# Kernel optimization log

Hardware: AMD Instinct MI355X
Metric: run time of the kernel (lower is better)

Reference implementation:

```python
import jax, jax.numpy as jnp
import numpy as np

C = 256  # in/feat/out channels
EPS = 1e-5

def layer_norm(x, g, b):
    mu = jnp.mean(x, axis=-1, keepdims=True)
    var = jnp.var(x, axis=-1, keepdims=True)
    return (x - mu) * jax.lax.rsqrt(var + EPS) * g + b

def setup_inputs() -> dict:
    key = jax.random.key(0)
    ks = jax.random.split(key, 16)
    N, K = 16384, 9
    s = 1.0 / np.sqrt(C)
    d = {
        "update_feature": jax.random.normal(ks[0], (N, C), jnp.float32),
        "input_feature": jax.random.normal(ks[1], (N, K, C), jnp.float32),
        "dyn_W": jax.random.uniform(ks[2], (2 * C, C), jnp.float32, -s, s),
        "dyn_b": jnp.zeros((2 * C,), jnp.float32),
        "inp_W": jax.random.uniform(ks[3], (2 * C, C), jnp.float32, -s, s),
        "inp_b": jnp.zeros((2 * C,), jnp.float32),
        "ig_W": jax.random.uniform(ks[4], (C, C), jnp.float32, -s, s),
        "ig_b": jnp.zeros((C,), jnp.float32),
        "ug_W": jax.random.uniform(ks[5], (C, C), jnp.float32, -s, s),
        "ug_b": jnp.zeros((C,), jnp.float32),
        "fc_W": jax.random.uniform(ks[6], (C, C), jnp.float32, -s, s),
        "fc_b": jnp.zeros((C,), jnp.float32),
        "norm_in_g": jnp.ones((C,), jnp.float32), "norm_in_b": jnp.zeros((C,), jnp.float32),
        "norm_out_g": jnp.ones((C,), jnp.float32), "norm_out_b": jnp.zeros((C,), jnp.float32),
        "inorm_in_g": jnp.ones((C,), jnp.float32), "inorm_in_b": jnp.zeros((C,), jnp.float32),
        "inorm_out_g": jnp.ones((C,), jnp.float32), "inorm_out_b": jnp.zeros((C,), jnp.float32),
        "fc_norm_g": jnp.ones((C,), jnp.float32), "fc_norm_b": jnp.zeros((C,), jnp.float32),
    }
    return d

def reference(update_feature, input_feature, dyn_W, dyn_b, inp_W, inp_b,
              ig_W, ig_b, ug_W, ug_b, fc_W, fc_b,
              norm_in_g, norm_in_b, norm_out_g, norm_out_b,
              inorm_in_g, inorm_in_b, inorm_out_g, inorm_out_b,
              fc_norm_g, fc_norm_b):
    uf = update_feature.reshape(-1, C)                     # [N, C]
    N = uf.shape[0]
    params = uf @ dyn_W.T + dyn_b                          # [N, 2C]
    param_in, param_out = params[:, :C], params[:, C:]
    inf = input_feature.reshape(N, -1, C)                  # [N, K, C]
    input_feats = jnp.einsum('nkc,dc->nkd', inf, inp_W) + inp_b  # [N, K, 2C]
    input_in, input_out = input_feats[..., :C], input_feats[..., C:]
    gate_feats = input_in * param_in[:, None, :]           # [N, K, C]
    input_gate = jax.nn.sigmoid(layer_norm(jnp.einsum('nkc,dc->nkd', gate_feats, ig_W) + ig_b, inorm_in_g, inorm_in_b))
    update_gate = jax.nn.sigmoid(layer_norm(jnp.einsum('nkc,dc->nkd', gate_feats, ug_W) + ug_b, norm_in_g, norm_in_b))
    param_out = layer_norm(param_out, norm_out_g, norm_out_b)
    input_out = layer_norm(input_out, inorm_out_g, inorm_out_b)
    features = update_gate * param_out[:, None, :] + input_gate * input_out
    features = jnp.einsum('nkc,dc->nkd', features, fc_W) + fc_b
    features = jax.nn.relu(layer_norm(features, fc_norm_g, fc_norm_b))
    return features
```

## Files before the change

### kernel.cpp

```cpp
#include <hip/hip_runtime.h>

#define EPS 1e-5f
#define APITCH 264

typedef __attribute__((ext_vector_type(8))) short bf16x8;
typedef __attribute__((ext_vector_type(4))) float f32x4;
typedef __attribute__((ext_vector_type(2))) float f32x2;

__device__ __forceinline__ unsigned short f2b_rtne(float f) {
  unsigned u = __builtin_bit_cast(unsigned, f);
  u += 0x7fffu + ((u >> 16) & 1u);
  return (unsigned short)(u >> 16);
}
__device__ __forceinline__ unsigned cvt_pk(float lo, float hi) {
  unsigned r;
  asm("v_cvt_pk_bf16_f32 %0, %1, %2" : "=v"(r) : "v"(lo), "v"(hi));
  return r;
}
__device__ __forceinline__ float bhalf(unsigned pk, int hi) {
  unsigned u = hi ? (pk & 0xffff0000u) : (pk << 16);
  return __builtin_bit_cast(float, u);
}
__device__ __forceinline__ int div9(int r) {
  return (int)(__umulhi((unsigned)r, 954437177u) >> 1);
}
__device__ __forceinline__ float fsig(float x) {
  return __builtin_amdgcn_rcpf(1.f + __expf(-x));
}

__device__ __forceinline__ f32x2 pk_add(f32x2 a, f32x2 b) {
  f32x2 d; asm("v_pk_add_f32 %0, %1, %2" : "=v"(d) : "v"(a), "v"(b)); return d;
}
__device__ __forceinline__ f32x2 pk_mul(f32x2 a, f32x2 b) {
  f32x2 d; asm("v_pk_mul_f32 %0, %1, %2" : "=v"(d) : "v"(a), "v"(b)); return d;
}
__device__ __forceinline__ f32x2 pk_fma(f32x2 a, f32x2 b, f32x2 c) {
  f32x2 d; asm("v_pk_fma_f32 %0, %1, %2, %3" : "=v"(d) : "v"(a), "v"(b), "v"(c)); return d;
}
__device__ __forceinline__ f32x2 ld2(const float* p) { return *(const f32x2*)p; }

template <int CTRL>
__device__ __forceinline__ float dppadd(float v) {
  int x = __builtin_amdgcn_update_dpp(0, __builtin_bit_cast(int, v), CTRL, 0xf, 0xf, true);
  return v + __builtin_bit_cast(float, x);
}
__device__ __forceinline__ float dpp_reduce16(float v) {
  v = dppadd<0xB1>(v);
  v = dppadd<0x4E>(v);
  v = dppadd<0x124>(v);
  v = dppadd<0x128>(v);
  return v;
}

__global__ void k_cvt_all(const float* __restrict__ dynW, const float* __restrict__ inpW,
                          const float* __restrict__ igW, const float* __restrict__ ugW,
                          const float* __restrict__ fcW, unsigned short* __restrict__ dst) {
  int i = blockIdx.x * blockDim.x + threadIdx.x;
  const float* src; int off; int perm;
  if (i < 131072)      { src = dynW; off = i;          perm = 0; }
  else if (i < 262144) { src = inpW; off = i - 131072; perm = 0; }
  else if (i < 327680) { src = igW;  off = i - 262144; perm = 1; }
  else if (i < 393216) { src = ugW;  off = i - 327680; perm = 1; }
  else                 { src = fcW;  off = i - 393216; perm = 1; }
  int j = off & 7, lane = (off >> 3) & 63, kk = (off >> 9) & 7, ct = off >> 12;
  int row = ct * 16 + (lane & 15);
  int p = kk * 32 + (lane >> 4) * 8 + j;
  int col = perm ? ((p & ~63) + (p & 3) * 16 + ((p >> 2) & 15)) : p;
  dst[i] = f2b_rtne(src[row * 256 + col]);
}


__device__ __forceinline__ void gemmQ(const short* src,
                                      const unsigned short* __restrict__ W,
                                      f32x4 (&acc)[4][2],
                                      int wv, int lane, int lr, int lh) {
#pragma unroll
  for (int q = 0; q < 4; q++) {
    const unsigned short* Wp = W + ((wv * 4 + q) << 12) + lane * 8;
    bf16x8 b[8];
#pragma unroll
    for (int kk = 0; kk < 8; kk++) b[kk] = *(const bf16x8*)&Wp[kk * 512];
    int zoff = 0;
    asm volatile("" : "+v"(zoff));
    const short* ap = src + zoff;
    bf16x8 a[8];
#pragma unroll
    for (int kk = 0; kk < 8; kk++)
      a[kk] = *(const bf16x8*)&ap[lr * APITCH + kk * 32 + lh * 8];
    acc[q][0] = (f32x4){0.f, 0.f, 0.f, 0.f};
#pragma unroll
    for (int kk = 0; kk < 8; kk++)
      acc[q][0] = __builtin_amdgcn_mfma_f32_16x16x32_bf16(a[kk], b[kk], acc[q][0], 0, 0, 0);
#pragma unroll
    for (int kk = 0; kk < 8; kk++)
      a[kk] = *(const bf16x8*)&ap[(16 + lr) * APITCH + kk * 32 + lh * 8];
    acc[q][1] = (f32x4){0.f, 0.f, 0.f, 0.f};
#pragma unroll
    for (int kk = 0; kk < 8; kk++)
      acc[q][1] = __builtin_amdgcn_mfma_f32_16x16x32_bf16(a[kk], b[kk], acc[q][1], 0, 0, 0);
  }
}

__device__ __forceinline__ void statsW(const f32x4 (&acc)[4][2], const f32x2 (&b42)[4],
                                       float* sP, float* qP, int wv, int lr, int lh) {
#pragma unroll
  for (int rh = 0; rh < 2; rh++)
#pragma unroll
    for (int p = 0; p < 2; p++) {
      f32x2 s2 = (f32x2){0.f, 0.f}, q2 = (f32x2){0.f, 0.f};
#pragma unroll
      for (int q = 0; q < 4; q++) {
        f32x2 a2 = (f32x2){acc[q][rh][2 * p], acc[q][rh][2 * p + 1]};
        f32x2 t = pk_add(a2, b42[q]);
        s2 = pk_add(s2, t);
        q2 = pk_fma(t, t, q2);
      }
      float s0 = dpp_reduce16(s2[0]);
      float s1 = dpp_reduce16(s2[1]);
      float q0 = dpp_reduce16(q2[0]);
      float q1 = dpp_reduce16(q2[1]);
      if (lr == 0) {
        int r = rh * 16 + lh * 4 + 2 * p;
        sP[wv * 32 + r] = s0;  sP[wv * 32 + r + 1] = s1;
        qP[wv * 32 + r] = q0;  qP[wv * 32 + r + 1] = q1;
      }
    }
}
__device__ __forceinline__ void statsR(const float* sP, const float* qP,
                                       f32x2 (&nmu)[2][2], f32x2 (&rv)[2][2], int lh) {
#pragma unroll
  for (int rh = 0; rh < 2; rh++)
#pragma unroll
    for (int p = 0; p < 2; p++) {
      int r = rh * 16 + lh * 4 + 2 * p;
      f32x2 S = pk_add(pk_add(ld2(sP + r), ld2(sP + 32 + r)),
                       pk_add(ld2(sP + 64 + r), ld2(sP + 96 + r)));
      f32x2 Q = pk_add(pk_add(ld2(qP + r), ld2(qP + 32 + r)),
                       pk_add(ld2(qP + 64 + r), ld2(qP + 96 + r)));
      float m0 = S[0] * (1.f / 256.f), m1 = S[1] * (1.f / 256.f);
      nmu[rh][p] = (f32x2){-m0, -m1};
      rv[rh][p] = (f32x2){rsqrtf(Q[0] * (1.f / 256.f) - m0 * m0 + EPS),
                          rsqrtf(Q[1] * (1.f / 256.f) - m1 * m1 + EPS)};
    }
}

__global__ __launch_bounds__(256) void k_main(
    const float* __restrict__ inf,
    const unsigned short* __restrict__ inpWf, const float* __restrict__ inpb,
    const unsigned short* __restrict__ igWf, const float* __restrict__ igb,
    const unsigned short* __restrict__ ugWf, const float* __restrict__ ugb,
    const unsigned short* __restrict__ fcWf, const float* __restrict__ fcb,
    const float* __restrict__ nig, const float* __restrict__ nib,
    const float* __restrict__ iig, const float* __restrict__ iib,
    const float* __restrict__ iog, const float* __restrict__ iob,
    const float* __restrict__ fng, const float* __restrict__ fnb,
    const float* __restrict__ param_in, const float* __restrict__ param_out_ln,
    float* __restrict__ out) {
  __shared__ short aT[32 * APITCH];
  __shared__ short gT[32 * APITCH];
  __shared__ float sP[2][128], qP[2][128];

  const int t = threadIdx.x;
  const int wv = t >> 6, lane = t & 63, lr = lane & 15, lh = lane >> 4;
  const int cb = wv * 64;
  const int r0 = blockIdx.x * 32;

#pragma unroll
  for (int j = 0; j < 8; j++) {
    const int idx4 = j * 256 + t;
    const int row = idx4 >> 6;
    const int c4 = (idx4 & 63) << 2;
    const float4 v = *(const float4*)&inf[(size_t)(r0 + row) * 256 + c4];
    uint2 pk;
    pk.x = cvt_pk(v.x, v.y);
    pk.y = cvt_pk(v.z, v.w);
    *(uint2*)&aT[row * APITCH + c4] = pk;
  }
  __syncthreads();

  f32x4 acc[4][2];
  f32x2 b42[4], ga2[4], be2[4], nmu[2][2], rv[2][2];
  unsigned gio[4][2][2];

  gemmQ(aT, inpWf, acc, wv, lane, lr, lh);
#pragma unroll
  for (int q = 0; q < 4; q++) { float b = inpb[cb + q * 16 + lr]; b42[q] = (f32x2){b, b}; }
#pragma unroll
  for (int rh = 0; rh < 2; rh++)
#pragma unroll
    for (int p = 0; p < 2; p++) {
      const int rrA = rh * 16 + lh * 4 + 2 * p;
      const float* pin0 = param_in + (size_t)div9(r0 + rrA) * 256;
      const float* pin1 = param_in + (size_t)div9(r0 + rrA + 1) * 256;
      float gAv[4], gBv[4];
#pragma unroll
      for (int q = 0; q < 4; q++) {
        f32x2 a2 = (f32x2){acc[q][rh][2 * p], acc[q][rh][2 * p + 1]};
        f32x2 tt = pk_add(a2, b42[q]);
        gAv[q] = tt[0] * pin0[cb + q * 16 + lr];
        gBv[q] = tt[1] * pin1[cb + q * 16 + lr];
      }
      uint2 pkA, pkB;
      pkA.x = cvt_pk(gAv[0], gAv[1]); pkA.y = cvt_pk(gAv[2], gAv[3]);
      pkB.x = cvt_pk(gBv[0], gBv[1]); pkB.y = cvt_pk(gBv[2], gBv[3]);
      *(uint2*)&gT[rrA * APITCH + cb + lr * 4] = pkA;
      *(uint2*)&gT[(rrA + 1) * APITCH + cb + lr * 4] = pkB;
    }

  gemmQ(aT, inpWf + (16 << 12), acc, wv, lane, lr, lh);
#pragma unroll
  for (int q = 0; q < 4; q++) { float b = inpb[256 + cb + q * 16 + lr]; b42[q] = (f32x2){b, b}; }
  statsW(acc, b42, sP[1], qP[1], wv, lr, lh);
  __syncthreads();
  statsR(sP[1], qP[1], nmu, rv, lh);
#pragma unroll
  for (int q = 0; q < 4; q++) {
    float g = iog[cb + q * 16 + lr], e = iob[cb + q * 16 + lr];
    ga2[q] = (f32x2){g, g}; be2[q] = (f32x2){e, e};
  }
#pragma unroll
  for (int q = 0; q < 4; q++)
#pragma unroll
    for (int rh = 0; rh < 2; rh++)
#pragma unroll
      for (int p = 0; p < 2; p++) {
        f32x2 a2 = (f32x2){acc[q][rh][2 * p], acc[q][rh][2 * p + 1]};
        f32x2 tt = pk_add(pk_add(a2, b42[q]), nmu[rh][p]);
        f32x2 v2 = pk_fma(pk_mul(tt, rv[rh][p]), ga2[q], be2[q]);
        gio[q][rh][p] = cvt_pk(v2[0], v2[1]);
      }

  gemmQ(gT, igWf, acc, wv, lane, lr, lh);
#pragma unroll
  for (int q = 0; q < 4; q++) { float b = igb[cb + q * 16 + lr]; b42[q] = (f32x2){b, b}; }
  statsW(acc, b42, sP[0], qP[0], wv, lr, lh);
  __syncthreads();
  statsR(sP[0], qP[0], nmu, rv, lh);
#pragma unroll
  for (int q = 0; q < 4; q++) {
    float g = iig[cb + q * 16 + lr], e = iib[cb + q * 16 + lr];
    ga2[q] = (f32x2){g, g}; be2[q] = (f32x2){e, e};
  }
#pragma unroll
  for (int q = 0; q < 4; q++)
#pragma unroll
    for (int rh = 0; rh < 2; rh++)
#pragma unroll
      for (int p = 0; p < 2; p++) {
        f32x2 a2 = (f32x2){acc[q][rh][2 * p], acc[q][rh][2 * p + 1]};
        f32x2 tt = pk_add(pk_add(a2, b42[q]), nmu[rh][p]);
        f32x2 p2 = pk_fma(pk_mul(tt, rv[rh][p]), ga2[q], be2[q]);
        float g10 = fsig(p2[0]);
        float g11 = fsig(p2[1]);
        unsigned w = gio[q][rh][p];
        gio[q][rh][p] = cvt_pk(g10 * bhalf(w, 0), g11 * bhalf(w, 1));
      }

  gemmQ(gT, ugWf, acc, wv, lane, lr, lh);
#pragma unroll
  for (int q = 0; q < 4; q++) { float b = ugb[cb + q * 16 + lr]; b42[q] = (f32x2){b, b}; }
  statsW(acc, b42, sP[1], qP[1], wv, lr, lh);
  __syncthreads();
  statsR(sP[1], qP[1], nmu, rv, lh);
#pragma unroll
  for (int q = 0; q < 4; q++) {
    float g = nig[cb + q * 16 + lr], e = nib[cb + q * 16 + lr];
    ga2[q] = (f32x2){g, g}; be2[q] = (f32x2){e, e};
  }
#pragma unroll
  for (int rh = 0; rh < 2; rh++)
#pragma unroll
    for (int p = 0; p < 2; p++) {
      const int rrA = rh * 16 + lh * 4 + 2 * p;
      const float* po0 = param_out_ln + (size_t)div9(r0 + rrA) * 256;
      const float* po1 = param_out_ln + (size_t)div9(r0 + rrA + 1) * 256;
      float fA[4], fB[4];
#pragma unroll
      for (int q = 0; q < 4; q++) {
        f32x2 a2 = (f32x2){acc[q][rh][2 * p], acc[q][rh][2 * p + 1]};
        f32x2 tt = pk_add(pk_add(a2, b42[q]), nmu[rh][p]);
        f32x2 u2 = pk_fma(pk_mul(tt, rv[rh][p]), ga2[q], be2[q]);
        float g20 = fsig(u2[0]);
        float g21 = fsig(u2[1]);
        unsigned w = gio[q][rh][p];
        fA[q] = g20 * po0[cb + q * 16 + lr] + bhalf(w, 0);
        fB[q] = g21 * po1[cb + q * 16 + lr] + bhalf(w, 1);
      }
      uint2 pkA, pkB;
      pkA.x = cvt_pk(fA[0], fA[1]); pkA.y = cvt_pk(fA[2], fA[3]);
      pkB.x = cvt_pk(fB[0], fB[1]); pkB.y = cvt_pk(fB[2], fB[3]);
      *(uint2*)&aT[rrA * APITCH + cb + lr * 4] = pkA;
      *(uint2*)&aT[(rrA + 1) * APITCH + cb + lr * 4] = pkB;
    }
  __syncthreads();

  gemmQ(aT, fcWf, acc, wv, lane, lr, lh);
#pragma unroll
  for (int q = 0; q < 4; q++) { float b = fcb[cb + q * 16 + lr]; b42[q] = (f32x2){b, b}; }
  statsW(acc, b42, sP[0], qP[0], wv, lr, lh);
  __syncthreads();
  statsR(sP[0], qP[0], nmu, rv, lh);
#pragma unroll
  for (int q = 0; q < 4; q++) {
    float g = fng[cb + q * 16 + lr], e = fnb[cb + q * 16 + lr];
    ga2[q] = (f32x2){g, g}; be2[q] = (f32x2){e, e};
  }
#pragma unroll
  for (int q = 0; q < 4; q++) {
    const int col = cb + q * 16 + lr;
#pragma unroll
    for (int rh = 0; rh < 2; rh++)
#pragma unroll
      for (int p = 0; p < 2; p++) {
        f32x2 a2 = (f32x2){acc[q][rh][2 * p], acc[q][rh][2 * p + 1]};
        f32x2 tt = pk_add(pk_add(a2, b42[q]), nmu[rh][p]);
        f32x2 v2 = pk_fma(pk_mul(tt, rv[rh][p]), ga2[q], be2[q]);
        const int rrA = r0 + rh * 16 + lh * 4 + 2 * p;
        out[(size_t)rrA * 256 + col] = fmaxf(v2[0], 0.f);
        out[(size_t)(rrA + 1) * 256 + col] = fmaxf(v2[1], 0.f);
      }
  }
}

#define FPITCH 516

__device__ __forceinline__ void red8(float& s, float& q) {
#pragma unroll
  for (int m = 1; m < 8; m <<= 1) { s += __shfl_xor(s, m); q += __shfl_xor(q, m); }
}

__global__ __launch_bounds__(256) void k_params(
    const float* __restrict__ uf, const unsigned short* __restrict__ dynWf,
    const float* __restrict__ dynb, const float* __restrict__ nog,
    const float* __restrict__ nob, float* __restrict__ param_in,
    float* __restrict__ param_out_ln) {
  __shared__ short aT[32 * APITCH];
  __shared__ float fBuf[32 * FPITCH];
  const int t = threadIdx.x;
  const int wv = t >> 6, lane = t & 63, lr = lane & 15, lh = lane >> 4;
  const int r0 = blockIdx.x * 32;
#pragma unroll
  for (int j = 0; j < 8; j++) {
    const int idx4 = j * 256 + t;
    const int row = idx4 >> 6;
    const int c4 = (idx4 & 63) << 2;
    const float4 v = *(const float4*)&uf[(size_t)(r0 + row) * 256 + c4];
    uint2 pk;
    pk.x = cvt_pk(v.x, v.y);
    pk.y = cvt_pk(v.z, v.w);
    *(uint2*)&aT[row * APITCH + c4] = pk;
  }
  __syncthreads();
  bf16x8 a0[8], a1[8];
#pragma unroll
  for (int kk = 0; kk < 8; kk++) {
    a0[kk] = *(const bf16x8*)&aT[lr * APITCH + kk * 32 + lh * 8];
    a1[kk] = *(const bf16x8*)&aT[(16 + lr) * APITCH + kk * 32 + lh * 8];
  }
#pragma unroll 1
  for (int cp = 0; cp < 8; cp++) {
    const int ct = wv * 8 + cp;
    bf16x8 b[8];
#pragma unroll
    for (int kk = 0; kk < 8; kk++)
      b[kk] = *(const bf16x8*)&dynWf[((ct * 8 + kk) * 64 + lane) * 8];
    const float bi = dynb[ct * 16 + lr];
    f32x4 c0 = {0.f, 0.f, 0.f, 0.f}, c1 = c0;
#pragma unroll
    for (int kk = 0; kk < 8; kk++) {
      c0 = __builtin_amdgcn_mfma_f32_16x16x32_bf16(a0[kk], b[kk], c0, 0, 0, 0);
      c1 = __builtin_amdgcn_mfma_f32_16x16x32_bf16(a1[kk], b[kk], c1, 0, 0, 0);
    }
#pragma unroll
    for (int i = 0; i < 4; i++) {
      fBuf[(lh * 4 + i) * FPITCH + ct * 16 + lr] = c0[i] + bi;
      fBuf[(16 + lh * 4 + i) * FPITCH + ct * 16 + lr] = c1[i] + bi;
    }
  }
  __syncthreads();
  const int row = t >> 3, j = t & 7;
  float s = 0.f, q = 0.f;
#pragma unroll
  for (int i = 0; i < 32; i++) {
    float x = fBuf[row * FPITCH + 256 + j + 8 * i];
    s += x; q += x * x;
  }
  red8(s, q);
  const float mu = s * (1.f / 256.f);
  const float rsv = rsqrtf(q * (1.f / 256.f) - mu * mu + EPS);
#pragma unroll 1
  for (int i = 0; i < 32; i++) {
    const int c = j + 8 * i;
    float x = fBuf[row * FPITCH + 256 + c];
    param_out_ln[(size_t)(r0 + row) * 256 + c] = (x - mu) * rsv * nog[c] + nob[c];
  }
#pragma unroll
  for (int jj = 0; jj < 8; jj++) {
    const int idx4 = jj * 256 + t;
    const int rwq = idx4 >> 6;
    const int c4 = (idx4 & 63) << 2;
    float4 v;
    v.x = fBuf[rwq * FPITCH + c4 + 0];
    v.y = fBuf[rwq * FPITCH + c4 + 1];
    v.z = fBuf[rwq * FPITCH + c4 + 2];
    v.w = fBuf[rwq * FPITCH + c4 + 3];
    *(float4*)&param_in[(size_t)(r0 + rwq) * 256 + c4] = v;
  }
}

extern "C" void kernel_launch(void* const* d_in, const int* in_sizes, int n_in,
                              void* d_out, int out_size, void* d_ws, size_t ws_size,
                              hipStream_t stream) {
  const float* uf   = (const float*)d_in[0];
  const float* inf  = (const float*)d_in[1];
  const float* dynW = (const float*)d_in[2];
  const float* dynb = (const float*)d_in[3];
  const float* inpW = (const float*)d_in[4];
  const float* inpb = (const float*)d_in[5];
  const float* igW  = (const float*)d_in[6];
  const float* igb  = (const float*)d_in[7];
  const float* ugW  = (const float*)d_in[8];
  const float* ugb  = (const float*)d_in[9];
  const float* fcW  = (const float*)d_in[10];
  const float* fcb  = (const float*)d_in[11];
  const float* nig  = (const float*)d_in[12];
  const float* nib  = (const float*)d_in[13];
  const float* nog  = (const float*)d_in[14];
  const float* nob  = (const float*)d_in[15];
  const float* iig  = (const float*)d_in[16];
  const float* iib  = (const float*)d_in[17];
  const float* iog  = (const float*)d_in[18];
  const float* iob  = (const float*)d_in[19];
  const float* fng  = (const float*)d_in[20];
  const float* fnb  = (const float*)d_in[21];
  float* out = (float*)d_out;

  char* ws = (char*)d_ws;
  unsigned short* Wf = (unsigned short*)ws;
  unsigned short* dynWf = Wf;
  unsigned short* inpWf = Wf + 131072;
  unsigned short* igWf  = Wf + 262144;
  unsigned short* ugWf  = Wf + 327680;
  unsigned short* fcWf  = Wf + 393216;
  float* param_in     = (float*)(ws + (1 << 20));
  float* param_out_ln = (float*)(ws + (1 << 20) + (16 << 20));

  k_cvt_all<<<dim3(1792), dim3(256), 0, stream>>>(dynW, inpW, igW, ugW, fcW, Wf);

  k_params<<<dim3(512), dim3(256), 0, stream>>>(uf, dynWf, dynb, nog, nob,
                                                param_in, param_out_ln);

  k_main<<<dim3(4608), dim3(256), 0, stream>>>(
      inf, inpWf, inpb, igWf, igb, ugWf, ugb, fcWf, fcb,
      nig, nib, iig, iib, iog, iob, fng, fnb,
      param_in, param_out_ln, out);
}
```

Before: 255.2 us.

## Store LDS activation tiles in MFMA fragment order instead of padded rows

Replaces the padded row-major LDS tiles (pitch 264) with a fragment-ordered layout so each lane reads its bf16x8 A operand at lane*8 + kk*512, which makes the reads contiguous and conflict-free. The stores of the gate and feature intermediates and the weight K-permutation in the conversion kernel are changed to match the new layout. This also shrinks LDS usage by dropping the padding. The cost is more complex index maths on the store side and a risk of layout mismatch or new bank conflicts on writes.

```diff
diff --git a/kernel.cpp b/kernel.cpp
--- a/kernel.cpp
+++ b/kernel.cpp
@@ -65,7 +65,13 @@
   int j = off & 7, lane = (off >> 3) & 63, kk = (off >> 9) & 7, ct = off >> 12;
   int row = ct * 16 + (lane & 15);
   int p = kk * 32 + (lane >> 4) * 8 + j;
-  int col = perm ? ((p & ~63) + (p & 3) * 16 + ((p >> 2) & 15)) : p;
+  int col;
+  if (perm) {
+    int q = p & 3, b0 = (p >> 2) & 1, lh4 = (p >> 3) & 3, kkp = p >> 5;
+    col = (kkp >> 1) * 64 + q * 16 + (kkp & 1) * 8 + lh4 * 2 + b0;
+  } else {
+    col = p;
+  }
   dst[i] = f2b_rtne(src[row * 256 + col]);
 }
 
@@ -73,7 +79,7 @@
 __device__ __forceinline__ void gemmQ(const short* src,
                                       const unsigned short* __restrict__ W,
                                       f32x4 (&acc)[4][2],
-                                      int wv, int lane, int lr, int lh) {
+                                      int wv, int lane) {
 #pragma unroll
   for (int q = 0; q < 4; q++) {
     const unsigned short* Wp = W + ((wv * 4 + q) << 12) + lane * 8;
@@ -82,18 +88,18 @@
     for (int kk = 0; kk < 8; kk++) b[kk] = *(const bf16x8*)&Wp[kk * 512];
     int zoff = 0;
     asm volatile("" : "+v"(zoff));
-    const short* ap = src + zoff;
+    const short* ap = src + zoff + lane * 8;
     bf16x8 a[8];
 #pragma unroll
     for (int kk = 0; kk < 8; kk++)
-      a[kk] = *(const bf16x8*)&ap[lr * APITCH + kk * 32 + lh * 8];
+      a[kk] = *(const bf16x8*)&ap[kk * 512];
     acc[q][0] = (f32x4){0.f, 0.f, 0.f, 0.f};
 #pragma unroll
     for (int kk = 0; kk < 8; kk++)
       acc[q][0] = __builtin_amdgcn_mfma_f32_16x16x32_bf16(a[kk], b[kk], acc[q][0], 0, 0, 0);
 #pragma unroll
     for (int kk = 0; kk < 8; kk++)
-      a[kk] = *(const bf16x8*)&ap[(16 + lr) * APITCH + kk * 32 + lh * 8];
+      a[kk] = *(const bf16x8*)&ap[4096 + kk * 512];
     acc[q][1] = (f32x4){0.f, 0.f, 0.f, 0.f};
 #pragma unroll
     for (int kk = 0; kk < 8; kk++)
@@ -156,8 +162,8 @@
     const float* __restrict__ fng, const float* __restrict__ fnb,
     const float* __restrict__ param_in, const float* __restrict__ param_out_ln,
     float* __restrict__ out) {
-  __shared__ short aT[32 * APITCH];
-  __shared__ short gT[32 * APITCH];
+  __shared__ short aT[32 * 256];
+  __shared__ short gT[32 * 256];
   __shared__ float sP[2][128], qP[2][128];
 
   const int t = threadIdx.x;
@@ -174,7 +180,9 @@
     uint2 pk;
     pk.x = cvt_pk(v.x, v.y);
     pk.y = cvt_pk(v.z, v.w);
-    *(uint2*)&aT[row * APITCH + c4] = pk;
+    const int sa = (row >> 4) * 4096 +
+                   (((c4 >> 5) * 64) + (row & 15) + ((c4 >> 3) & 3) * 16) * 8 + (c4 & 7);
+    *(uint2*)&aT[sa] = pk;
   }
   __syncthreads();
 
@@ -182,7 +190,11 @@
   f32x2 b42[4], ga2[4], be2[4], nmu[2][2], rv[2][2];
   unsigned gio[4][2][2];
 
-  gemmQ(aT, inpWf, acc, wv, lane, lr, lh);
+  const int kkp = 2 * wv + (lr >> 3);
+  const int lh4 = (lr >> 1) & 3;
+  const int jb = (lr & 1) * 4;
+
+  gemmQ(aT, inpWf, acc, wv, lane);
 #pragma unroll
   for (int q = 0; q < 4; q++) { float b = inpb[cb + q * 16 + lr]; b42[q] = (f32x2){b, b}; }
 #pragma unroll
@@ -203,11 +215,12 @@
       uint2 pkA, pkB;
       pkA.x = cvt_pk(gAv[0], gAv[1]); pkA.y = cvt_pk(gAv[2], gAv[3]);
       pkB.x = cvt_pk(gBv[0], gBv[1]); pkB.y = cvt_pk(gBv[2], gBv[3]);
-      *(uint2*)&gT[rrA * APITCH + cb + lr * 4] = pkA;
-      *(uint2*)&gT[(rrA + 1) * APITCH + cb + lr * 4] = pkB;
-    }
-
-  gemmQ(aT, inpWf + (16 << 12), acc, wv, lane, lr, lh);
+      const int base = rh * 4096 + (kkp * 64 + lh * 4 + 2 * p + lh4 * 16) * 8 + jb;
+      *(uint2*)&gT[base] = pkA;
+      *(uint2*)&gT[base + 8] = pkB;
+    }
+
+  gemmQ(aT, inpWf + (16 << 12), acc, wv, lane);
 #pragma unroll
   for (int q = 0; q < 4; q++) { float b = inpb[256 + cb + q * 16 + lr]; b42[q] = (f32x2){b, b}; }
   statsW(acc, b42, sP[1], qP[1], wv, lr, lh);
@@ -230,7 +243,7 @@
         gio[q][rh][p] = cvt_pk(v2[0], v2[1]);
       }
 
-  gemmQ(gT, igWf, acc, wv, lane, lr, lh);
+  gemmQ(gT, igWf, acc, wv, lane);
 #pragma unroll
   for (int q = 0; q < 4; q++) { float b = igb[cb + q * 16 + lr]; b42[q] = (f32x2){b, b}; }
   statsW(acc, b42, sP[0], qP[0], wv, lr, lh);
@@ -256,7 +269,7 @@
         gio[q][rh][p] = cvt_pk(g10 * bhalf(w, 0), g11 * bhalf(w, 1));
       }
 
-  gemmQ(gT, ugWf, acc, wv, lane, lr, lh);
+  gemmQ(gT, ugWf, acc, wv, lane);
 #pragma unroll
   for (int q = 0; q < 4; q++) { float b = ugb[cb + q * 16 + lr]; b42[q] = (f32x2){b, b}; }
   statsW(acc, b42, sP[1], qP[1], wv, lr, lh);
@@ -289,12 +302,13 @@
       uint2 pkA, pkB;
       pkA.x = cvt_pk(fA[0], fA[1]); pkA.y = cvt_pk(fA[2], fA[3]);
       pkB.x = cvt_pk(fB[0], fB[1]); pkB.y = cvt_pk(fB[2], fB[3]);
-      *(uint2*)&aT[rrA * APITCH + cb + lr * 4] = pkA;
-      *(uint2*)&aT[(rrA + 1) * APITCH + cb + lr * 4] = pkB;
-    }
-  __syncthreads();
-
-  gemmQ(aT, fcWf, acc, wv, lane, lr, lh);
+      const int base = rh * 4096 + (kkp * 64 + lh * 4 + 2 * p + lh4 * 16) * 8 + jb;
+      *(uint2*)&aT[base] = pkA;
+      *(uint2*)&aT[base + 8] = pkB;
+    }
+  __syncthreads();
+
+  gemmQ(aT, fcWf, acc, wv, lane);
 #pragma unroll
   for (int q = 0; q < 4; q++) { float b = fcb[cb + q * 16 + lr]; b42[q] = (f32x2){b, b}; }
   statsW(acc, b42, sP[0], qP[0], wv, lr, lh);
```

New measurement: 252.4 us, median of 2. Within noise of the previous version (-1.1%).
